# Optimization experiments

Measured on AMD Instinct MI355X. Metric: run time of the kernel, lower is better.

Reference implementation:

```python
import jax, jax.numpy as jnp
import numpy as np

N, D, P, H = 4096, 128, 128, 256  # n samples, input_dim, pe_dim, hidden_dim


def setup_inputs() -> dict:
    key = jax.random.key(0)
    k0, k1, k2 = jax.random.split(key, 3)
    x = jax.random.normal(k0, (N, D), dtype=jnp.float32)
    # shared_net params: Linear(D+P -> H), Linear(H -> 1)
    W1 = jax.random.normal(k1, (D + P, H), dtype=jnp.float32) / np.sqrt(D + P).astype(np.float32)
    b1 = jnp.zeros((H,), dtype=jnp.float32)
    W2 = jax.random.normal(k2, (H, 1), dtype=jnp.float32) / np.sqrt(H).astype(np.float32)
    b2 = jnp.zeros((1,), dtype=jnp.float32)
    return {"x": x, "W1": W1, "b1": b1, "W2": W2, "b2": b2}


def reference(x, W1, b1, W2, b2):
    """Vectorized NIMO.forward: all d feature-masked MLP evals in one batched GEMM.

    Original python loop: for each j, zero column j of x, append one-hot pe[:, :P],
    run shared MLP -> g_j (n,), column j of B is x[:, j] * (1 + g_j).
    Output B has shape (n, d+1) with a leading ones column.
    Dropout(noise_std=0.0) is identity.
    """
    n, d = x.shape
    p = W1.shape[0] - d
    dt = x.dtype
    # (d, n, d): x replicated d times with column j zeroed in slice j
    mask = (1.0 - jnp.eye(d)).astype(dt)
    x_masked = x[None, :, :] * mask[:, None, :]
    # First linear layer, split into masked-x part and (constant per j) pe part.
    h = jnp.einsum('jni,ih->jnh', x_masked, W1[:d])          # (d, n, h)
    pe_add = jnp.eye(d, dtype=dt)[:, :p] @ W1[d:]            # (d, h): one-hot pe through W1
    h = jax.nn.relu(h + pe_add[:, None, :] + b1)
    g = jnp.einsum('jnh,ho->jno', h, W2)[..., 0] + b2[0]     # (d, n)
    cols = x * (1.0 + g.T)                                   # (n, d)
    return jnp.concatenate([jnp.ones((n, 1), dtype=dt), cols], axis=1)  # (n, d+1)
```

## Files before the change

kernel.cpp:

```cpp
#include <hip/hip_runtime.h>


#define NROWS 4096
#define DIN   128
#define HDIM  256
#define JCH   8

typedef float sfloat16 __attribute__((ext_vector_type(16)));

__global__ __launch_bounds__(256) void nimo_base(
    const float* __restrict__ x, const float* __restrict__ W1,
    const float* __restrict__ b1, float* __restrict__ baseb)
{
    __shared__ float xs[DIN * 36];
    const int tid  = threadIdx.x;
    const int row0 = blockIdx.x * 32;
    const int h0   = blockIdx.y * 64;

    {
        const int bidx = tid * 16;
        const int r = bidx >> 7;
        const int c = bidx & 127;
        #pragma unroll
        for (int u = 0; u < 4; ++u) {
            const float4 v = *(const float4*)(x + (size_t)(row0 + r) * DIN + c + u * 4);
            xs[(c + u * 4 + 0) * 36 + r] = v.x;
            xs[(c + u * 4 + 1) * 36 + r] = v.y;
            xs[(c + u * 4 + 2) * 36 + r] = v.z;
            xs[(c + u * 4 + 3) * 36 + r] = v.w;
        }
    }
    __syncthreads();

    const int tx = tid & 31;
    const int ty = tid >> 5;
    const float* __restrict__ wcol = W1 + h0 + tx * 2;

    float2 acc[4];
    #pragma unroll
    for (int u = 0; u < 4; ++u) { acc[u].x = 0.f; acc[u].y = 0.f; }

    #pragma unroll 8
    for (int k = 0; k < DIN; ++k) {
        const float2 w  = *(const float2*)(wcol + (size_t)k * HDIM);
        const float4 xv = *(const float4*)(&xs[k * 36 + ty * 4]);
        acc[0].x = fmaf(xv.x, w.x, acc[0].x); acc[0].y = fmaf(xv.x, w.y, acc[0].y);
        acc[1].x = fmaf(xv.y, w.x, acc[1].x); acc[1].y = fmaf(xv.y, w.y, acc[1].y);
        acc[2].x = fmaf(xv.z, w.x, acc[2].x); acc[2].y = fmaf(xv.z, w.y, acc[2].y);
        acc[3].x = fmaf(xv.w, w.x, acc[3].x); acc[3].y = fmaf(xv.w, w.y, acc[3].y);
    }

    const float2 bv = *(const float2*)(b1 + h0 + tx * 2);
    #pragma unroll
    for (int u = 0; u < 4; ++u) {
        float2 o; o.x = acc[u].x + bv.x; o.y = acc[u].y + bv.y;
        *(float2*)(baseb + (size_t)(row0 + ty * 4 + u) * HDIM + h0 + tx * 2) = o;
    }
}

__global__ __launch_bounds__(1024, 8) void nimo_main(
    const float* __restrict__ x, const float* __restrict__ W1,
    const float* __restrict__ W2, const float* __restrict__ b2,
    const float* __restrict__ baseb, float* __restrict__ out)
{
    __shared__ float xs[64][JCH + 1];
    __shared__ float part[16][JCH][66];

    const int tid  = threadIdx.x;
    const int r    = tid & 63;
    const int q    = tid >> 6;
    const int row0 = blockIdx.x * 64;
    const int row  = row0 + r;
    const int j0   = blockIdx.y * JCH;
    const int h0   = q * 16;

    if (tid < 512) {
        const int xr = tid >> 3;
        const int xc = tid & 7;
        xs[xr][xc] = x[(size_t)(row0 + xr) * DIN + j0 + xc];
    }

    float bb[16], w2r[16];
    {
        const float4* bp  = (const float4*)(baseb + (size_t)row * HDIM + h0);
        const float4* wp2 = (const float4*)(W2 + h0);
        #pragma unroll
        for (int u = 0; u < 4; ++u) {
            const float4 v = bp[u];
            bb[u * 4 + 0] = v.x; bb[u * 4 + 1] = v.y;
            bb[u * 4 + 2] = v.z; bb[u * 4 + 3] = v.w;
            const float4 w = wp2[u];
            w2r[u * 4 + 0] = w.x; w2r[u * 4 + 1] = w.y;
            w2r[u * 4 + 2] = w.z; w2r[u * 4 + 3] = w.w;
        }
    }
    __syncthreads();

    for (int jj = 0; jj < JCH; ++jj) {
        const float xj = xs[r][jj];
        unsigned off = (unsigned)(((j0 + jj) * HDIM + h0) * 4);
        off = __builtin_amdgcn_readfirstlane(off);
        sfloat16 wa, wp;
        asm volatile(
            "s_load_dwordx16 %0, %2, 0x0\n\t"
            "s_load_dwordx16 %1, %2, 0x20000\n\t"
            "s_waitcnt lgkmcnt(0)"
            : "=s"(wa), "=s"(wp)
            : "s"((unsigned long long)(uintptr_t)W1 + off));

        float acc = 0.f;
        #pragma unroll
        for (int h = 0; h < 16; ++h) {
            float t = bb[h] + wp[h];
            t = fmaf(-xj, wa[h], t);
            t = fmaxf(t, 0.f);
            acc = fmaf(t, w2r[h], acc);
        }
        part[q][jj][r] = acc;
    }
    __syncthreads();

    const float b2s = b2[0];
    if (blockIdx.y == 0 && tid < 64) out[(size_t)(row0 + tid) * 129] = 1.0f;

    if (tid < 512) {
        const int rr = tid >> 3;
        const int jj = tid & 7;
        float g = 0.f;
        #pragma unroll
        for (int qq = 0; qq < 16; ++qq) g += part[qq][jj][rr];
        const float xv = xs[rr][jj];
        out[(size_t)(row0 + rr) * 129 + 1 + j0 + jj] = xv * (1.0f + g + b2s);
    }
}

extern "C" void kernel_launch(void* const* d_in, const int* in_sizes, int n_in,
                              void* d_out, int out_size, void* d_ws, size_t ws_size,
                              hipStream_t stream) {
    const float* x  = (const float*)d_in[0];
    const float* W1 = (const float*)d_in[1];
    const float* b1 = (const float*)d_in[2];
    const float* W2 = (const float*)d_in[3];
    const float* b2 = (const float*)d_in[4];
    float* out = (float*)d_out;
    float* baseb = (float*)d_ws;

    nimo_base<<<dim3(NROWS / 32, HDIM / 64), 256, 0, stream>>>(x, W1, b1, baseb);
    nimo_main<<<dim3(NROWS / 64, DIN / JCH), 1024, 0, stream>>>(x, W1, W2, b2, baseb, out);
}
```

Baseline: 88.02 us.

## Use packed fp16 math with fdot2 and stage W1 rows in LDS

The main kernel's inner loop now runs in packed half precision: base activations, W1 rows and W2 are converted to fp16, the add/fma/relu run as 2-wide vector ops, and the W2 reduction uses fdot2 into an fp32 accumulator. The W1 rows for the block's column chunk, plus their positional-encoding counterparts, are staged once in LDS as fp16 instead of being fetched per iteration with scalar loads. This halves the VALU instruction count and removes the scalar-load wait inside the loop. The cost is reduced precision in the hidden activations, which may exceed the accuracy tolerance, and some extra LDS traffic.

```diff
diff --git a/kernel.cpp b/kernel.cpp
--- a/kernel.cpp
+++ b/kernel.cpp
@@ -6,7 +6,11 @@
 #define HDIM  256
 #define JCH   8
 
-typedef float sfloat16 __attribute__((ext_vector_type(16)));
+typedef _Float16 h2 __attribute__((ext_vector_type(2)));
+
+static __device__ __forceinline__ h2 mk_h2(float a, float b) {
+    h2 r; r[0] = (_Float16)a; r[1] = (_Float16)b; return r;
+}
 
 __global__ __launch_bounds__(256) void nimo_base(
     const float* __restrict__ x, const float* __restrict__ W1,
@@ -65,6 +69,7 @@
 {
     __shared__ float xs[64][JCH + 1];
     __shared__ float part[16][JCH][66];
+    __shared__ __align__(16) _Float16 w1s[16][HDIM];
 
     const int tid  = threadIdx.x;
     const int r    = tid & 63;
@@ -80,42 +85,58 @@
         xs[xr][xc] = x[(size_t)(row0 + xr) * DIN + j0 + xc];
     }
 
-    float bb[16], w2r[16];
     {
-        const float4* bp  = (const float4*)(baseb + (size_t)row * HDIM + h0);
+        const int rl = tid >> 7;
+        const int c2 = (tid & 127) * 2;
+        const float* wr = W1 + (size_t)(j0 + rl) * HDIM + c2;
+        *(h2*)&w1s[rl][c2] = mk_h2(wr[0], wr[1]);
+        const float* wr2 = W1 + (size_t)(DIN + j0 + rl) * HDIM + c2;
+        *(h2*)&w1s[8 + rl][c2] = mk_h2(wr2[0], wr2[1]);
+    }
+
+    h2 bbh[8], w2h[8];
+    {
+        const float4* bp = (const float4*)(baseb + (size_t)row * HDIM + h0);
+        const float4 v0 = bp[0], v1 = bp[1], v2 = bp[2], v3 = bp[3];
+        bbh[0] = mk_h2(v0.x, v0.y); bbh[1] = mk_h2(v0.z, v0.w);
+        bbh[2] = mk_h2(v1.x, v1.y); bbh[3] = mk_h2(v1.z, v1.w);
+        bbh[4] = mk_h2(v2.x, v2.y); bbh[5] = mk_h2(v2.z, v2.w);
+        bbh[6] = mk_h2(v3.x, v3.y); bbh[7] = mk_h2(v3.z, v3.w);
         const float4* wp2 = (const float4*)(W2 + h0);
-        #pragma unroll
-        for (int u = 0; u < 4; ++u) {
-            const float4 v = bp[u];
-            bb[u * 4 + 0] = v.x; bb[u * 4 + 1] = v.y;
-            bb[u * 4 + 2] = v.z; bb[u * 4 + 3] = v.w;
-            const float4 w = wp2[u];
-            w2r[u * 4 + 0] = w.x; w2r[u * 4 + 1] = w.y;
-            w2r[u * 4 + 2] = w.z; w2r[u * 4 + 3] = w.w;
-        }
+        const float4 u0 = wp2[0], u1 = wp2[1], u2 = wp2[2], u3 = wp2[3];
+        w2h[0] = mk_h2(u0.x, u0.y); w2h[1] = mk_h2(u0.z, u0.w);
+        w2h[2] = mk_h2(u1.x, u1.y); w2h[3] = mk_h2(u1.z, u1.w);
+        w2h[4] = mk_h2(u2.x, u2.y); w2h[5] = mk_h2(u2.z, u2.w);
+        w2h[6] = mk_h2(u3.x, u3.y); w2h[7] = mk_h2(u3.z, u3.w);
     }
     __syncthreads();
 
+    h2 z2; z2[0] = (_Float16)0.f; z2[1] = (_Float16)0.f;
+
     for (int jj = 0; jj < JCH; ++jj) {
         const float xj = xs[r][jj];
-        unsigned off = (unsigned)(((j0 + jj) * HDIM + h0) * 4);
-        off = __builtin_amdgcn_readfirstlane(off);
-        sfloat16 wa, wp;
-        asm volatile(
-            "s_load_dwordx16 %0, %2, 0x0\n\t"
-            "s_load_dwordx16 %1, %2, 0x20000\n\t"
-            "s_waitcnt lgkmcnt(0)"
-            : "=s"(wa), "=s"(wp)
-            : "s"((unsigned long long)(uintptr_t)W1 + off));
+        const _Float16 nv = (_Float16)(-xj);
+        h2 nx2; nx2[0] = nv; nx2[1] = nv;
+
+        const uint4 wa_lo = *(const uint4*)&w1s[jj][h0];
+        const uint4 wa_hi = *(const uint4*)&w1s[jj][h0 + 8];
+        const uint4 wp_lo = *(const uint4*)&w1s[8 + jj][h0];
+        const uint4 wp_hi = *(const uint4*)&w1s[8 + jj][h0 + 8];
 
         float acc = 0.f;
-        #pragma unroll
-        for (int h = 0; h < 16; ++h) {
-            float t = bb[h] + wp[h];
-            t = fmaf(-xj, wa[h], t);
-            t = fmaxf(t, 0.f);
-            acc = fmaf(t, w2r[h], acc);
-        }
+        #define STEP(P, WAU, WPU) { \
+            const h2 wa = __builtin_bit_cast(h2, WAU); \
+            const h2 wp = __builtin_bit_cast(h2, WPU); \
+            h2 t = bbh[P] + wp;                       \
+            t = nx2 * wa + t;                         \
+            t = __builtin_elementwise_max(t, z2);     \
+            acc = __builtin_amdgcn_fdot2(t, w2h[P], acc, false); }
+        STEP(0, wa_lo.x, wp_lo.x) STEP(1, wa_lo.y, wp_lo.y)
+        STEP(2, wa_lo.z, wp_lo.z) STEP(3, wa_lo.w, wp_lo.w)
+        STEP(4, wa_hi.x, wp_hi.x) STEP(5, wa_hi.y, wp_hi.y)
+        STEP(6, wa_hi.z, wp_hi.z) STEP(7, wa_hi.w, wp_hi.w)
+        #undef STEP
+
         part[q][jj][r] = acc;
     }
     __syncthreads();
```

After: 87.95 us. No clear change (-0.1%).
